# Optimization experiments

Hardware: AMD Instinct MI355X
Metric: run time of the kernel (lower is better)

The kernel has to match this reference:

```python
import jax, jax.numpy as jnp
import numpy as np

B, T, C = 2, 2048, 1024
H = 16
DH = C // H  # 64
EPS = 1e-5


def setup_inputs() -> dict:
    key = jax.random.key(0)
    ks = jax.random.split(key, 12)
    s = lambda k, shape, fan: jax.random.normal(k, shape, jnp.float32) / np.sqrt(fan)
    return {
        'x': jax.random.normal(ks[0], (B, T, C), jnp.float32),
        'wq': s(ks[1], (H, C, DH), C),
        'wk': s(ks[2], (H, C, DH), C),
        'wv': s(ks[3], (H, C, DH), C),
        'w_proj': s(ks[4], (C, C), C),
        'b_proj': jnp.zeros((C,), jnp.float32),
        'g_ln1': jnp.ones((C,), jnp.float32),
        'b_ln1': jnp.zeros((C,), jnp.float32),
        'g_ln2': jnp.ones((C,), jnp.float32),
        'b_ln2': jnp.zeros((C,), jnp.float32),
        'w_ff1': s(ks[5], (C, 4 * C), C),
        'b_ff1': jnp.zeros((4 * C,), jnp.float32),
        'w_ff2': s(ks[6], (4 * C, C), 4 * C),
        'b_ff2': jnp.zeros((C,), jnp.float32),
    }


def _layernorm(x, g, b):
    mu = jnp.mean(x, axis=-1, keepdims=True)
    var = jnp.mean(jnp.square(x - mu), axis=-1, keepdims=True)
    return (x - mu) * jax.lax.rsqrt(var + EPS) * g + b


def _attention(x, wq, wk, wv, w_proj, b_proj):
    # per-head projections, batched over heads: [B,T,C] x [H,C,Dh] -> [B,H,T,Dh]
    q = jnp.einsum('btc,hcd->bhtd', x, wq)
    k = jnp.einsum('btc,hcd->bhtd', x, wk)
    v = jnp.einsum('btc,hcd->bhtd', x, wv)
    scores = jnp.einsum('bhtd,bhsd->bhts', q, k) / np.sqrt(DH).astype(np.float32)
    t = x.shape[1]
    causal = jnp.tril(jnp.ones((t, t), bool))
    scores = jnp.where(causal, scores, -jnp.inf)
    w = jax.nn.softmax(scores, axis=-1)
    out = jnp.einsum('bhts,bhsd->bhtd', w, v)  # [B,H,T,Dh]
    # concat heads (head order matches torch cat over head list)
    out = out.transpose(0, 2, 1, 3).reshape(x.shape[0], t, C)
    return out @ w_proj + b_proj


def reference(x, wq, wk, wv, w_proj, b_proj, g_ln1, b_ln1, g_ln2, b_ln2, w_ff1, b_ff1, w_ff2, b_ff2):
    x = x + _attention(_layernorm(x, g_ln1, b_ln1), wq, wk, wv, w_proj, b_proj)
    h = _layernorm(x, g_ln2, b_ln2)
    ff = jax.nn.relu(h @ w_ff1 + b_ff1) @ w_ff2 + b_ff2
    return x + ff
```

## Files before the change

### kernel.cpp

```cpp
#include <hip/hip_runtime.h>

#define DEV __device__ __forceinline__

typedef __attribute__((ext_vector_type(4))) float f32x4;
typedef __attribute__((ext_vector_type(8))) short short8;
typedef __attribute__((ext_vector_type(8))) __bf16 bf16x8;

DEV unsigned short f2bf(float f) {
  unsigned u = __builtin_bit_cast(unsigned, f);
  u += 0x7fffu + ((u >> 16) & 1u);
  return (unsigned short)(u >> 16);
}
DEV unsigned pack2(float a, float b) {
  return (unsigned)f2bf(a) | ((unsigned)f2bf(b) << 16);
}
DEV bf16x8 ld_bf8(const unsigned short* p) {
  short8 v = *(const short8*)p;
  return __builtin_bit_cast(bf16x8, v);
}
DEV f32x4 MFMA(bf16x8 a, bf16x8 b, f32x4 c) {
  return __builtin_amdgcn_mfma_f32_16x16x32_bf16(a, b, c, 0, 0, 0);
}

typedef const __attribute__((address_space(1))) void GV;
typedef __attribute__((address_space(3))) void LV;
DEV void gl_lds16(const void* g, void* l) {
  __builtin_amdgcn_global_load_lds((GV*)g, (LV*)l, 16, 0, 0);
}

DEV void xcd_decode(int gx, int& bx, int& by) {
  const int nwg = gridDim.x, bid = blockIdx.x;
  const int cpx = nwg >> 3;
  const int swz = (bid & 7) * cpx + (bid >> 3);
  by = swz / gx;
  bx = swz % gx;
}

__global__ void __launch_bounds__(256) ln_fused(
    const float* __restrict__ x, const float* __restrict__ g,
    const float* __restrict__ b, unsigned short* __restrict__ y)
{
  const int row = blockIdx.x, tid = threadIdx.x;
  const float4 xv = ((const float4*)(x + (size_t)row * 1024))[tid];
  float s  = xv.x + xv.y + xv.z + xv.w;
  float s2 = xv.x * xv.x + xv.y * xv.y + xv.z * xv.z + xv.w * xv.w;
#pragma unroll
  for (int o = 32; o > 0; o >>= 1) { s += __shfl_down(s, o); s2 += __shfl_down(s2, o); }
  __shared__ float ps[4], ps2[4];
  if ((tid & 63) == 0) { ps[tid >> 6] = s; ps2[tid >> 6] = s2; }
  __syncthreads();
  float S  = ps[0] + ps[1] + ps[2] + ps[3];
  float S2 = ps2[0] + ps2[1] + ps2[2] + ps2[3];
  float mu = S * (1.f / 1024.f);
  float rs = rsqrtf(S2 * (1.f / 1024.f) - mu * mu + 1e-5f);
  const float4 gv = ((const float4*)g)[tid];
  const float4 bv = ((const float4*)b)[tid];
  uint2 r;
  r.x = pack2((xv.x - mu) * rs * gv.x + bv.x, (xv.y - mu) * rs * gv.y + bv.y);
  r.y = pack2((xv.z - mu) * rs * gv.z + bv.z, (xv.w - mu) * rs * gv.w + bv.w);
  ((uint2*)(y + (size_t)row * 1024))[tid] = r;
}

__global__ void __launch_bounds__(256) transp_f2b(
    const float* __restrict__ src, unsigned short* __restrict__ dst, int R, int C)
{
  __shared__ float t[64][65];
  const int c0 = blockIdx.x * 64, r0 = blockIdx.y * 64;
  const int tx = threadIdx.x & 63, tq = threadIdx.x >> 6;
#pragma unroll
  for (int i = 0; i < 16; i++) {
    int r = tq * 16 + i;
    t[r][tx] = src[(size_t)(r0 + r) * C + c0 + tx];
  }
  __syncthreads();
#pragma unroll
  for (int i = 0; i < 16; i++) {
    int c = tq * 16 + i;
    dst[(size_t)(c0 + c) * R + r0 + tx] = f2bf(t[tx][c]);
  }
}

__global__ void __launch_bounds__(256) qkv_transp(
    const float* __restrict__ wq, const float* __restrict__ wk,
    const float* __restrict__ wv, unsigned short* __restrict__ dst)
{
  __shared__ float t[64][65];
  const int c0 = blockIdx.x * 64, h = blockIdx.y, z = blockIdx.z;
  const float* w = (z == 0 ? wq : z == 1 ? wk : wv) + (size_t)h * 1024 * 64;
  const int tx = threadIdx.x & 63, tq = threadIdx.x >> 6;
#pragma unroll
  for (int i = 0; i < 16; i++) {
    int c = tq * 16 + i;
    t[c][tx] = w[(size_t)(c0 + c) * 64 + tx];
  }
  __syncthreads();
  unsigned short* drow = dst + (size_t)(z * 1024 + h * 64) * 1024 + c0;
#pragma unroll
  for (int i = 0; i < 16; i++) {
    int d = tq * 16 + i;
    drow[(size_t)d * 1024 + tx] = f2bf(t[tx][d]);
  }
}

__global__ void __launch_bounds__(256) v_transp(
    const unsigned short* __restrict__ qkv, unsigned short* __restrict__ vt)
{
  __shared__ unsigned s[64][65];
  const int t0 = blockIdx.x * 64, h = blockIdx.y, b = blockIdx.z;
  const int tx = threadIdx.x & 63, tq = threadIdx.x >> 6;
#pragma unroll
  for (int i = 0; i < 16; i++) {
    int tr = tq * 16 + i;
    s[tr][tx] = qkv[(size_t)(b * 2048 + t0 + tr) * 3072 + 2048 + h * 64 + tx];
  }
  __syncthreads();
  unsigned short* vb = vt + (size_t)((b * 16 + h) * 64) * 2048 + t0;
#pragma unroll
  for (int i = 0; i < 16; i++) {
    int d = tq * 16 + i;
    vb[(size_t)d * 2048 + tx] = (unsigned short)s[tx][d];
  }
}

template<int BIAS, int RELU, int RES, int OBF>
__global__ void __launch_bounds__(256) gemm_bt(
    const unsigned short* __restrict__ A, const unsigned short* __restrict__ Bt,
    const float* __restrict__ bias, const float* __restrict__ res,
    void* __restrict__ out, int M, int N, int K, int gx)
{
  __shared__ unsigned short As[128 * 32];
  __shared__ unsigned short Bs[128 * 32];
  int bx, by;
  xcd_decode(gx, bx, by);
  const int tid = threadIdx.x;
  const int wid = tid >> 6, lane = tid & 63;
  const int lg = lane >> 4, lr = lane & 15;
  const int m0 = by * 128, n0 = bx * 128;
  const int wr = (wid >> 1) * 64, wc = (wid & 1) * 64;

  const unsigned short* ga = A + (size_t)(m0 + (tid >> 2)) * K + (tid & 3) * 8;
  const unsigned short* gb = Bt + (size_t)(n0 + (tid >> 2)) * K + (tid & 3) * 8;
  char* asb = (char*)As + wid * 1024;
  char* bsb = (char*)Bs + wid * 1024;

  f32x4 acc[4][4] = {};

  for (int k0 = 0; k0 < K; k0 += 32) {
    gl_lds16(ga + k0, asb);
    gl_lds16(ga + k0 + (size_t)64 * K, asb + 4096);
    gl_lds16(gb + k0, bsb);
    gl_lds16(gb + k0 + (size_t)64 * K, bsb + 4096);
    __syncthreads();
    bf16x8 a[4], b[4];
#pragma unroll
    for (int m = 0; m < 4; m++) a[m] = ld_bf8(&As[(wr + m * 16 + lr) * 32 + lg * 8]);
#pragma unroll
    for (int n = 0; n < 4; n++) b[n] = ld_bf8(&Bs[(wc + n * 16 + lr) * 32 + lg * 8]);
#pragma unroll
    for (int m = 0; m < 4; m++)
#pragma unroll
      for (int n = 0; n < 4; n++)
        acc[m][n] = MFMA(a[m], b[n], acc[m][n]);
    __syncthreads();
  }

#pragma unroll
  for (int m = 0; m < 4; m++) {
    const int row0 = m0 + wr + m * 16 + lg * 4;
#pragma unroll
    for (int n = 0; n < 4; n++) {
      const int col = n0 + wc + n * 16 + lr;
      const float bv = BIAS ? bias[col] : 0.f;
#pragma unroll
      for (int r = 0; r < 4; r++) {
        const size_t off = (size_t)(row0 + r) * N + col;
        float v = acc[m][n][r] + bv;
        if (RES) v += res[off];
        if (RELU) v = v > 0.f ? v : 0.f;
        if (OBF) ((unsigned short*)out)[off] = f2bf(v);
        else     ((float*)out)[off] = v;
      }
    }
  }
}

template<int BIAS, int RELU, int RES, int OBF>
__global__ void __launch_bounds__(256) gemm_bt64(
    const unsigned short* __restrict__ A, const unsigned short* __restrict__ Bt,
    const float* __restrict__ bias, const float* __restrict__ res,
    void* __restrict__ out, int M, int N, int K, int gx)
{
  __shared__ unsigned short As[64 * 32];
  __shared__ unsigned short Bs[128 * 32];
  int bx, by;
  xcd_decode(gx, bx, by);
  const int tid = threadIdx.x;
  const int wid = tid >> 6, lane = tid & 63;
  const int lg = lane >> 4, lr = lane & 15;
  const int m0 = by * 64, n0 = bx * 128;
  const int wr = (wid >> 1) * 32, wc = (wid & 1) * 64;

  const unsigned short* ga = A + (size_t)(m0 + (tid >> 2)) * K + (tid & 3) * 8;
  const unsigned short* gb = Bt + (size_t)(n0 + (tid >> 2)) * K + (tid & 3) * 8;
  char* asb = (char*)As + wid * 1024;
  char* bsb = (char*)Bs + wid * 1024;

  f32x4 acc[2][4] = {};

  for (int k0 = 0; k0 < K; k0 += 32) {
    gl_lds16(ga + k0, asb);
    gl_lds16(gb + k0, bsb);
    gl_lds16(gb + k0 + (size_t)64 * K, bsb + 4096);
    __syncthreads();
    bf16x8 a[2], b[4];
#pragma unroll
    for (int m = 0; m < 2; m++) a[m] = ld_bf8(&As[(wr + m * 16 + lr) * 32 + lg * 8]);
#pragma unroll
    for (int n = 0; n < 4; n++) b[n] = ld_bf8(&Bs[(wc + n * 16 + lr) * 32 + lg * 8]);
#pragma unroll
    for (int m = 0; m < 2; m++)
#pragma unroll
      for (int n = 0; n < 4; n++)
        acc[m][n] = MFMA(a[m], b[n], acc[m][n]);
    __syncthreads();
  }

#pragma unroll
  for (int m = 0; m < 2; m++) {
    const int row0 = m0 + wr + m * 16 + lg * 4;
#pragma unroll
    for (int n = 0; n < 4; n++) {
      const int col = n0 + wc + n * 16 + lr;
      const float bv = BIAS ? bias[col] : 0.f;
#pragma unroll
      for (int r = 0; r < 4; r++) {
        const size_t off = (size_t)(row0 + r) * N + col;
        float v = acc[m][n][r] + bv;
        if (RES) v += res[off];
        if (RELU) v = v > 0.f ? v : 0.f;
        if (OBF) ((unsigned short*)out)[off] = f2bf(v);
        else     ((float*)out)[off] = v;
      }
    }
  }
}

__global__ void __launch_bounds__(256) attn_fwd(
    const unsigned short* __restrict__ qkv, const unsigned short* __restrict__ vt,
    unsigned short* __restrict__ out)
{
  __shared__ unsigned short Ks[2][64 * 64];
  __shared__ unsigned short Vs[2][64 * 64];
  __shared__ unsigned short P[4][16][72];

  const int j  = blockIdx.x;
  const int bh = blockIdx.y;
  const int b = bh >> 4, h = bh & 15;
  const int tid = threadIdx.x, wid = tid >> 6, lane = tid & 63;
  const int lg = lane >> 4, lr = lane & 15;

  const int tA = j, tB = 31 - j;
  const int nkt = tB + 1;

  const unsigned short* kbase = qkv + (size_t)(b * 2048) * 3072 + 1024 + h * 64;
  const unsigned short* vbase = vt + (size_t)(bh * 64) * 2048;

  const int sr = tid >> 3;
  const int sc = tid & 7;
  const int c0 = sc ^ (sr & 7);

  auto stage = [&](int buf, int kt) {
    const int kv0 = kt * 64;
    char* kd = (char*)&Ks[buf][0] + wid * 1024;
    char* vd = (char*)&Vs[buf][0] + wid * 1024;
    gl_lds16(kbase + (size_t)(kv0 + sr) * 3072 + c0 * 8, kd);
    gl_lds16(kbase + (size_t)(kv0 + 32 + sr) * 3072 + c0 * 8, kd + 4096);
    gl_lds16(vbase + (size_t)sr * 2048 + kv0 + c0 * 8, vd);
    gl_lds16(vbase + (size_t)(32 + sr) * 2048 + kv0 + c0 * 8, vd + 4096);
  };

  auto process = [&](int kt, int qt, const bf16x8& qf0, const bf16x8& qf1,
                     f32x4 (&o)[4], float& m, float& l, int buf) {
    const int kv0 = kt * 64;
    const int qg = qt * 64 + wid * 16 + lr;
    const unsigned short* Kb = &Ks[buf][0];
    const unsigned short* Vb = &Vs[buf][0];
    f32x4 s[4] = {};
    __builtin_amdgcn_s_setprio(1);
#pragma unroll
    for (int f = 0; f < 4; f++) {
      const int row = f * 16 + lr;
      const int rc = row & 7;
      s[f] = MFMA(ld_bf8(Kb + row * 64 + (lg ^ rc) * 8), qf0, s[f]);
      s[f] = MFMA(ld_bf8(Kb + row * 64 + ((lg | 4) ^ rc) * 8), qf1, s[f]);
    }
    __builtin_amdgcn_s_setprio(0);
    float p[16];
    float mt = -1e30f;
    const bool diag = (kt == qt);
#pragma unroll
    for (int f = 0; f < 4; f++)
#pragma unroll
      for (int r = 0; r < 4; r++) {
        float sv = s[f][r] * 0.125f;
        if (diag) {
          const int kv = kv0 + f * 16 + lg * 4 + r;
          sv = (kv <= qg) ? sv : -1e30f;
        }
        p[f * 4 + r] = sv;
        mt = fmaxf(mt, sv);
      }
    mt = fmaxf(mt, __shfl_xor(mt, 16));
    mt = fmaxf(mt, __shfl_xor(mt, 32));
    const float mnew = fmaxf(m, mt);
    const float sf = __expf(m - mnew);
    m = mnew;
    float ps = 0.f;
#pragma unroll
    for (int i = 0; i < 16; i++) { p[i] = __expf(p[i] - mnew); ps += p[i]; }
    ps += __shfl_xor(ps, 16);
    ps += __shfl_xor(ps, 32);
    l = l * sf + ps;
#pragma unroll
    for (int df = 0; df < 4; df++) o[df] *= sf;
    unsigned short* Pr = &P[wid][lr][0];
#pragma unroll
    for (int f = 0; f < 4; f++) {
      *(unsigned*)(Pr + f * 16 + lg * 4)     = pack2(p[f * 4 + 0], p[f * 4 + 1]);
      *(unsigned*)(Pr + f * 16 + lg * 4 + 2) = pack2(p[f * 4 + 2], p[f * 4 + 3]);
    }
    const bf16x8 pf0 = ld_bf8(Pr + lg * 8);
    const bf16x8 pf1 = ld_bf8(Pr + 32 + lg * 8);
    __builtin_amdgcn_s_setprio(1);
#pragma unroll
    for (int df = 0; df < 4; df++) {
      const int row = df * 16 + lr;
      const int rc = row & 7;
      o[df] = MFMA(ld_bf8(Vb + row * 64 + (lg ^ rc) * 8), pf0, o[df]);
      o[df] = MFMA(ld_bf8(Vb + row * 64 + ((lg | 4) ^ rc) * 8), pf1, o[df]);
    }
    __builtin_amdgcn_s_setprio(0);
  };

  const unsigned short* qb = qkv + (size_t)(b * 2048) * 3072 + h * 64;
  const int qrA = tA * 64 + wid * 16 + lr;
  const int qrB = tB * 64 + wid * 16 + lr;
  const bf16x8 qA0 = ld_bf8(qb + (size_t)qrA * 3072 + lg * 8);
  const bf16x8 qA1 = ld_bf8(qb + (size_t)qrA * 3072 + 32 + lg * 8);
  const bf16x8 qB0 = ld_bf8(qb + (size_t)qrB * 3072 + lg * 8);
  const bf16x8 qB1 = ld_bf8(qb + (size_t)qrB * 3072 + 32 + lg * 8);

  f32x4 oA[4] = {}, oB[4] = {};
  float mA = -1e30f, lA = 0.f, mB = -1e30f, lB = 0.f;

  stage(0, 0);
  __syncthreads();
  for (int kt = 0; kt < nkt; kt++) {
    const int buf = kt & 1;
    if (kt + 1 < nkt) stage(buf ^ 1, kt + 1);
    if (kt <= tA) process(kt, tA, qA0, qA1, oA, mA, lA, buf);
    process(kt, tB, qB0, qB1, oB, mB, lB, buf);
    __syncthreads();
  }

  const float invA = 1.f / lA, invB = 1.f / lB;
  {
    const int qg = tA * 64 + wid * 16 + lr;
    unsigned* orow = (unsigned*)(out + (size_t)(b * 2048 + qg) * 1024 + h * 64 + lg * 4);
#pragma unroll
    for (int df = 0; df < 4; df++) {
      orow[df * 8 + 0] = pack2(oA[df][0] * invA, oA[df][1] * invA);
      orow[df * 8 + 1] = pack2(oA[df][2] * invA, oA[df][3] * invA);
    }
  }
  {
    const int qg = tB * 64 + wid * 16 + lr;
    unsigned* orow = (unsigned*)(out + (size_t)(b * 2048 + qg) * 1024 + h * 64 + lg * 4);
#pragma unroll
    for (int df = 0; df < 4; df++) {
      orow[df * 8 + 0] = pack2(oB[df][0] * invB, oB[df][1] * invB);
      orow[df * 8 + 1] = pack2(oB[df][2] * invB, oB[df][3] * invB);
    }
  }
}

extern "C" void kernel_launch(void* const* d_in, const int* in_sizes, int n_in,
                              void* d_out, int out_size, void* d_ws, size_t ws_size,
                              hipStream_t stream)
{
  const float* x     = (const float*)d_in[0];
  const float* wq    = (const float*)d_in[1];
  const float* wk    = (const float*)d_in[2];
  const float* wv    = (const float*)d_in[3];
  const float* wproj = (const float*)d_in[4];
  const float* bproj = (const float*)d_in[5];
  const float* gln1  = (const float*)d_in[6];
  const float* bln1  = (const float*)d_in[7];
  const float* gln2  = (const float*)d_in[8];
  const float* bln2  = (const float*)d_in[9];
  const float* wff1  = (const float*)d_in[10];
  const float* bff1  = (const float*)d_in[11];
  const float* wff2  = (const float*)d_in[12];
  const float* bff2  = (const float*)d_in[13];

  char* ws = (char*)d_ws;
  const size_t MB = 1u << 20;
  float*          x2    = (float*)         (ws + 0 * MB);
  unsigned short* hbuf  = (unsigned short*)(ws + 16 * MB);
  unsigned short* xn1   = (unsigned short*)(ws + 24 * MB);
  unsigned short* attn  = (unsigned short*)(ws + 24 * MB);
  unsigned short* qkvb  = (unsigned short*)(ws + 32 * MB);
  unsigned short* vtb   = (unsigned short*)(ws + 56 * MB);
  unsigned short* a1    = (unsigned short*)(ws + 32 * MB);
  unsigned short* wqkvT = (unsigned short*)(ws + 64 * MB);
  unsigned short* wprojT= (unsigned short*)(ws + 70 * MB);
  unsigned short* wff1T = (unsigned short*)(ws + 72 * MB);
  unsigned short* wff2T = (unsigned short*)(ws + 80 * MB);

  qkv_transp<<<dim3(16, 16, 3), 256, 0, stream>>>(wq, wk, wv, wqkvT);
  transp_f2b<<<dim3(16, 16), 256, 0, stream>>>(wproj, wprojT, 1024, 1024);
  transp_f2b<<<dim3(64, 16), 256, 0, stream>>>(wff1, wff1T, 1024, 4096);
  transp_f2b<<<dim3(16, 64), 256, 0, stream>>>(wff2, wff2T, 4096, 1024);

  ln_fused<<<4096, 256, 0, stream>>>(x, gln1, bln1, xn1);
  gemm_bt<0, 0, 0, 1><<<768, 256, 0, stream>>>(
      xn1, wqkvT, nullptr, nullptr, qkvb, 4096, 3072, 1024, 24);
  v_transp<<<dim3(32, 16, 2), 256, 0, stream>>>(qkvb, vtb);
  attn_fwd<<<dim3(16, 32), 256, 0, stream>>>(qkvb, vtb, attn);
  gemm_bt64<1, 0, 1, 0><<<512, 256, 0, stream>>>(
      attn, wprojT, bproj, x, x2, 4096, 1024, 1024, 8);
  ln_fused<<<4096, 256, 0, stream>>>(x2, gln2, bln2, hbuf);
  gemm_bt<1, 1, 0, 1><<<1024, 256, 0, stream>>>(
      hbuf, wff1T, bff1, nullptr, a1, 4096, 4096, 1024, 32);
  gemm_bt64<1, 0, 1, 0><<<512, 256, 0, stream>>>(
      a1, wff2T, bff2, x2, (float*)d_out, 4096, 1024, 4096, 8);
}
```

Baseline: 279.2 us.

## Double-buffer LDS in GEMM kernels with XOR swizzle and wider K tile

Both bf16 GEMM kernels now keep two LDS buffers: the next K tile is loaded from global memory while MFMAs run on the current one, and one barrier per iteration replaces two. LDS columns are XOR-swizzled on both the global-to-LDS stores and the fragment reads to cut bank conflicts. The 64-row kernel also widens its K step from 32 to 64, halving loop iterations. This doubles LDS use per block, which may lower occupancy. The single barrier relies on the prefetch being issued after the sync, so the buffer it writes was last read in the previous iteration.

```diff
diff --git a/kernel.cpp b/kernel.cpp
--- a/kernel.cpp
+++ b/kernel.cpp
@@ -128,8 +128,8 @@
     const float* __restrict__ bias, const float* __restrict__ res,
     void* __restrict__ out, int M, int N, int K, int gx)
 {
-  __shared__ unsigned short As[128 * 32];
-  __shared__ unsigned short Bs[128 * 32];
+  __shared__ unsigned short As[2][128 * 32];
+  __shared__ unsigned short Bs[2][128 * 32];
   int bx, by;
   xcd_decode(gx, bx, by);
   const int tid = threadIdx.x;
@@ -138,30 +138,39 @@
   const int m0 = by * 128, n0 = bx * 128;
   const int wr = (wid >> 1) * 64, wc = (wid & 1) * 64;
 
-  const unsigned short* ga = A + (size_t)(m0 + (tid >> 2)) * K + (tid & 3) * 8;
-  const unsigned short* gb = Bt + (size_t)(n0 + (tid >> 2)) * K + (tid & 3) * 8;
-  char* asb = (char*)As + wid * 1024;
-  char* bsb = (char*)Bs + wid * 1024;
+  const int srow = tid >> 2;
+  const int scs = (tid & 3) ^ (srow & 3);
+  const unsigned short* ga = A + (size_t)(m0 + srow) * K + scs * 8;
+  const unsigned short* gb = Bt + (size_t)(n0 + srow) * K + scs * 8;
+  const int ca = (lg ^ (lr & 3)) * 8;
 
   f32x4 acc[4][4] = {};
 
-  for (int k0 = 0; k0 < K; k0 += 32) {
+  auto stage = [&](int buf, int k0) {
+    char* asb = (char*)&As[buf][0] + wid * 1024;
+    char* bsb = (char*)&Bs[buf][0] + wid * 1024;
     gl_lds16(ga + k0, asb);
     gl_lds16(ga + k0 + (size_t)64 * K, asb + 4096);
     gl_lds16(gb + k0, bsb);
     gl_lds16(gb + k0 + (size_t)64 * K, bsb + 4096);
+  };
+
+  stage(0, 0);
+  int cur = 0;
+  for (int k0 = 0; k0 < K; k0 += 32) {
     __syncthreads();
+    if (k0 + 32 < K) stage(cur ^ 1, k0 + 32);
     bf16x8 a[4], b[4];
 #pragma unroll
-    for (int m = 0; m < 4; m++) a[m] = ld_bf8(&As[(wr + m * 16 + lr) * 32 + lg * 8]);
-#pragma unroll
-    for (int n = 0; n < 4; n++) b[n] = ld_bf8(&Bs[(wc + n * 16 + lr) * 32 + lg * 8]);
+    for (int m = 0; m < 4; m++) a[m] = ld_bf8(&As[cur][(wr + m * 16 + lr) * 32 + ca]);
+#pragma unroll
+    for (int n = 0; n < 4; n++) b[n] = ld_bf8(&Bs[cur][(wc + n * 16 + lr) * 32 + ca]);
 #pragma unroll
     for (int m = 0; m < 4; m++)
 #pragma unroll
       for (int n = 0; n < 4; n++)
         acc[m][n] = MFMA(a[m], b[n], acc[m][n]);
-    __syncthreads();
+    cur ^= 1;
   }
 
 #pragma unroll
@@ -190,8 +199,8 @@
     const float* __restrict__ bias, const float* __restrict__ res,
     void* __restrict__ out, int M, int N, int K, int gx)
 {
-  __shared__ unsigned short As[64 * 32];
-  __shared__ unsigned short Bs[128 * 32];
+  __shared__ unsigned short As[2][64 * 64];
+  __shared__ unsigned short Bs[2][128 * 64];
   int bx, by;
   xcd_decode(gx, bx, by);
   const int tid = threadIdx.x;
@@ -200,29 +209,47 @@
   const int m0 = by * 64, n0 = bx * 128;
   const int wr = (wid >> 1) * 32, wc = (wid & 1) * 64;
 
-  const unsigned short* ga = A + (size_t)(m0 + (tid >> 2)) * K + (tid & 3) * 8;
-  const unsigned short* gb = Bt + (size_t)(n0 + (tid >> 2)) * K + (tid & 3) * 8;
-  char* asb = (char*)As + wid * 1024;
-  char* bsb = (char*)Bs + wid * 1024;
+  const int srow = tid >> 3;
+  const int scs = (tid & 7) ^ (srow & 7);
+  const unsigned short* ga = A + (size_t)(m0 + srow) * K + scs * 8;
+  const unsigned short* gb = Bt + (size_t)(n0 + srow) * K + scs * 8;
+  const int lxs = lr & 7;
 
   f32x4 acc[2][4] = {};
 
-  for (int k0 = 0; k0 < K; k0 += 32) {
+  auto stage = [&](int buf, int k0) {
+    char* asb = (char*)&As[buf][0] + wid * 1024;
+    char* bsb = (char*)&Bs[buf][0] + wid * 1024;
     gl_lds16(ga + k0, asb);
+    gl_lds16(ga + k0 + (size_t)32 * K, asb + 4096);
     gl_lds16(gb + k0, bsb);
-    gl_lds16(gb + k0 + (size_t)64 * K, bsb + 4096);
+    gl_lds16(gb + k0 + (size_t)32 * K, bsb + 4096);
+    gl_lds16(gb + k0 + (size_t)64 * K, bsb + 8192);
+    gl_lds16(gb + k0 + (size_t)96 * K, bsb + 12288);
+  };
+
+  stage(0, 0);
+  int cur = 0;
+  for (int k0 = 0; k0 < K; k0 += 64) {
     __syncthreads();
-    bf16x8 a[2], b[4];
-#pragma unroll
-    for (int m = 0; m < 2; m++) a[m] = ld_bf8(&As[(wr + m * 16 + lr) * 32 + lg * 8]);
-#pragma unroll
-    for (int n = 0; n < 4; n++) b[n] = ld_bf8(&Bs[(wc + n * 16 + lr) * 32 + lg * 8]);
-#pragma unroll
-    for (int m = 0; m < 2; m++)
+    if (k0 + 64 < K) stage(cur ^ 1, k0 + 64);
+#pragma unroll
+    for (int kk = 0; kk < 2; kk++) {
+      const int cb = kk * 4;
+      bf16x8 a[2], b[4];
+#pragma unroll
+      for (int m = 0; m < 2; m++)
+        a[m] = ld_bf8(&As[cur][(wr + m * 16 + lr) * 64 + ((cb + lg) ^ lxs) * 8]);
 #pragma unroll
       for (int n = 0; n < 4; n++)
-        acc[m][n] = MFMA(a[m], b[n], acc[m][n]);
-    __syncthreads();
+        b[n] = ld_bf8(&Bs[cur][(wc + n * 16 + lr) * 64 + ((cb + lg) ^ lxs) * 8]);
+#pragma unroll
+      for (int m = 0; m < 2; m++)
+#pragma unroll
+        for (int n = 0; n < 4; n++)
+          acc[m][n] = MFMA(a[m], b[n], acc[m][n]);
+    }
+    cur ^= 1;
   }
 
 #pragma unroll
```

After: 260.6 us. 6.6% less time.
